# Kernel tuning notes

Measured on AMD Instinct MI355X. Metric: run time of the kernel, lower is better.

Reference implementation:

```python
import jax, jax.numpy as jnp
import numpy as np
from jax import lax

T, D, NH, CATS = 1024, 2048, 2048, 1000


def setup_inputs() -> dict:
    key = jax.random.key(0)
    ks = jax.random.split(key, 16)
    s = 0.02
    return {
        "x": jax.random.normal(ks[0], (T, D), dtype=jnp.float32),
        "Wh": jax.random.normal(ks[1], (NH, D), dtype=jnp.float32) * s,
        "Wz": jax.random.normal(ks[2], (NH, D), dtype=jnp.float32) * s,
        "Wr": jax.random.normal(ks[3], (NH, D), dtype=jnp.float32) * s,
        "Uh": jax.random.normal(ks[4], (NH, NH), dtype=jnp.float32) * s,
        "Uz": jax.random.normal(ks[5], (NH, NH), dtype=jnp.float32) * s,
        "bz": jax.random.normal(ks[6], (NH,), dtype=jnp.float32) * s,
        "Ur": jax.random.normal(ks[7], (NH, NH), dtype=jnp.float32) * s,
        "br": jax.random.normal(ks[8], (NH,), dtype=jnp.float32) * s,
        "Wout": jax.random.normal(ks[9], (CATS, NH), dtype=jnp.float32) * s,
        "h0": jax.random.normal(ks[10], (NH,), dtype=jnp.float32),
        "zt0": jax.random.normal(ks[11], (NH,), dtype=jnp.float32),
        "htilde0": jax.random.normal(ks[12], (NH,), dtype=jnp.float32),
        "hprev0": jax.random.normal(ks[13], (NH,), dtype=jnp.float32),
    }


def reference(x, Wh, Wz, Wr, Uh, Uz, bz, Ur, br, Wout, h0, zt0, htilde0, hprev0):
    # Batch the input projections over all timesteps: [T,d] @ [d,nh] -> [T,nh]
    xh = x @ Wh.T
    xz = x @ Wz.T
    xr = x @ Wr.T

    # Faithful to the original update ORDER: h is computed from the *stale*
    # zt/htilde (from the previous iteration), then gates are refreshed.
    # The original's hadamard(a, b) = linear(a, diag(b)) is exactly a * b.
    def step(carry, xs):
        h, zt, htilde, hprev = carry
        xh_t, xz_t, xr_t = xs
        h_new = (1.0 - zt) * hprev + zt * htilde
        zt_new = jax.nn.sigmoid(xz_t + hprev @ Uz.T + bz)
        htilde_new = jnp.tanh(xh_t + hprev @ Uh.T)
        # rt = sigmoid(xr_t + hprev @ Ur.T + br)  # computed in original, never used
        return (h_new, zt_new, htilde_new, h_new), None

    (h_fin, _, _, _), _ = lax.scan(step, (h0, zt0, htilde0, hprev0), (xh, xz, xr))
    logits = h_fin @ Wout.T  # [cats]
    return jax.nn.softmax(logits, axis=0)
```

## Files before the change

kernel.cpp:

```cpp
#include <hip/hip_runtime.h>
#include <math.h>

#define TT  1024
#define DD  2048
#define NHH 2048
#define CC  1000

__global__ __launch_bounds__(256) void k_gemm(const float* __restrict__ X,
                                              const float* __restrict__ Wh,
                                              const float* __restrict__ Wz,
                                              const float* __restrict__ bz,
                                              float* __restrict__ XH,
                                              float* __restrict__ XZ) {
    __shared__ float As[32][68];
    __shared__ float Bs[32][68];
    const int z = blockIdx.z;
    const float* __restrict__ W = z ? Wz : Wh;
    float* __restrict__ OUT = z ? XZ : XH;
    const int n0 = blockIdx.x * 64;
    const int m0 = blockIdx.y * 64;
    const int tid = threadIdx.x;
    const int tx = tid & 15, ty = tid >> 4;
    const int lr = tid >> 2;
    const int lc = (tid & 3) * 8;

    float acc[4][4] = {};
    for (int k0 = 0; k0 < DD; k0 += 32) {
        float4 a0 = *(const float4*)&X[(size_t)(m0 + lr) * DD + k0 + lc];
        float4 a1 = *(const float4*)&X[(size_t)(m0 + lr) * DD + k0 + lc + 4];
        float4 b0 = *(const float4*)&W[(size_t)(n0 + lr) * DD + k0 + lc];
        float4 b1 = *(const float4*)&W[(size_t)(n0 + lr) * DD + k0 + lc + 4];
        As[lc+0][lr]=a0.x; As[lc+1][lr]=a0.y; As[lc+2][lr]=a0.z; As[lc+3][lr]=a0.w;
        As[lc+4][lr]=a1.x; As[lc+5][lr]=a1.y; As[lc+6][lr]=a1.z; As[lc+7][lr]=a1.w;
        Bs[lc+0][lr]=b0.x; Bs[lc+1][lr]=b0.y; Bs[lc+2][lr]=b0.z; Bs[lc+3][lr]=b0.w;
        Bs[lc+4][lr]=b1.x; Bs[lc+5][lr]=b1.y; Bs[lc+6][lr]=b1.z; Bs[lc+7][lr]=b1.w;
        __syncthreads();
#pragma unroll
        for (int kk = 0; kk < 32; ++kk) {
            float4 av = *(const float4*)&As[kk][ty * 4];
            float4 bv = *(const float4*)&Bs[kk][tx * 4];
            acc[0][0] = fmaf(av.x, bv.x, acc[0][0]); acc[0][1] = fmaf(av.x, bv.y, acc[0][1]);
            acc[0][2] = fmaf(av.x, bv.z, acc[0][2]); acc[0][3] = fmaf(av.x, bv.w, acc[0][3]);
            acc[1][0] = fmaf(av.y, bv.x, acc[1][0]); acc[1][1] = fmaf(av.y, bv.y, acc[1][1]);
            acc[1][2] = fmaf(av.y, bv.z, acc[1][2]); acc[1][3] = fmaf(av.y, bv.w, acc[1][3]);
            acc[2][0] = fmaf(av.z, bv.x, acc[2][0]); acc[2][1] = fmaf(av.z, bv.y, acc[2][1]);
            acc[2][2] = fmaf(av.z, bv.z, acc[2][2]); acc[2][3] = fmaf(av.z, bv.w, acc[2][3]);
            acc[3][0] = fmaf(av.w, bv.x, acc[3][0]); acc[3][1] = fmaf(av.w, bv.y, acc[3][1]);
            acc[3][2] = fmaf(av.w, bv.z, acc[3][2]); acc[3][3] = fmaf(av.w, bv.w, acc[3][3]);
        }
        __syncthreads();
    }
    float4 bias = make_float4(0.f, 0.f, 0.f, 0.f);
    if (z) bias = *(const float4*)&bz[n0 + tx * 4];
#pragma unroll
    for (int i = 0; i < 4; ++i) {
        float4 o = make_float4(acc[i][0] + bias.x, acc[i][1] + bias.y,
                               acc[i][2] + bias.z, acc[i][3] + bias.w);
        *(float4*)&OUT[(size_t)(m0 + ty * 4 + i) * NHH + n0 + tx * 4] = o;
    }
}

__global__ __launch_bounds__(256, 1) void k_recur(
    const float* __restrict__ XH, const float* __restrict__ XZ,
    const float* __restrict__ Uh, const float* __restrict__ Uz,
    const float* __restrict__ zt0, const float* __restrict__ ht0,
    const float* __restrict__ hp0,
    unsigned long long* __restrict__ Hbuf) {
    __shared__ float Hs[NHH];
    __shared__ float dot_s[16];
    const int tid  = threadIdx.x;
    const int wave = tid >> 6, lane = tid & 63;
    const int base8 = blockIdx.x * 8;

    const float* __restrict__ Um = (wave < 2) ? Uz : Uh;
    const int r0 = base8 + (wave & 1) * 4;
    float u[4][32];
#pragma unroll
    for (int r = 0; r < 4; ++r) {
        const float* __restrict__ row = Um + (size_t)(r0 + r) * NHH;
#pragma unroll
        for (int c = 0; c < 8; ++c) {
            float4 v = *(const float4*)&row[c * 256 + lane * 4];
            u[r][c*4+0] = v.x; u[r][c*4+1] = v.y; u[r][c*4+2] = v.z; u[r][c*4+3] = v.w;
        }
    }
#pragma unroll
    for (int k = 0; k < 8; ++k) Hs[k * 256 + tid] = hp0[k * 256 + tid];

    float p_cur = 0.f;
    if (tid < 8) {
        float z0 = zt0[base8 + tid], g0 = ht0[base8 + tid], p0 = hp0[base8 + tid];
        p_cur = (1.0f - z0) * p0 + z0 * g0;
        unsigned long long pr = (1ull << 32) | (unsigned long long)__float_as_uint(p_cur);
        __hip_atomic_store(&Hbuf[(size_t)1 * NHH + base8 + tid], pr,
                           __ATOMIC_RELAXED, __HIP_MEMORY_SCOPE_SYSTEM);
    }
    __syncthreads();

    for (int t = 1; t < TT; ++t) {
        const unsigned long long* __restrict__ src = Hbuf + (size_t)(t & 3) * NHH;
        unsigned long long pv[8];
#pragma unroll
        for (int k = 0; k < 8; ++k)
            pv[k] = __hip_atomic_load(&src[k * 256 + tid], __ATOMIC_RELAXED, __HIP_MEMORY_SCOPE_SYSTEM);
        float xzv = 0.f, xhv = 0.f;
        if (tid < 8) {
            xzv = XZ[(size_t)(t - 1) * NHH + base8 + tid];
            xhv = XH[(size_t)(t - 1) * NHH + base8 + tid];
        }
        float a0 = 0.f, a1 = 0.f, a2 = 0.f, a3 = 0.f;
#pragma unroll
        for (int c = 0; c < 8; ++c) {
            float4 h4 = *(const float4*)&Hs[c * 256 + lane * 4];
            a0 = fmaf(u[0][c*4+0], h4.x, fmaf(u[0][c*4+1], h4.y, fmaf(u[0][c*4+2], h4.z, fmaf(u[0][c*4+3], h4.w, a0))));
            a1 = fmaf(u[1][c*4+0], h4.x, fmaf(u[1][c*4+1], h4.y, fmaf(u[1][c*4+2], h4.z, fmaf(u[1][c*4+3], h4.w, a1))));
            a2 = fmaf(u[2][c*4+0], h4.x, fmaf(u[2][c*4+1], h4.y, fmaf(u[2][c*4+2], h4.z, fmaf(u[2][c*4+3], h4.w, a2))));
            a3 = fmaf(u[3][c*4+0], h4.x, fmaf(u[3][c*4+1], h4.y, fmaf(u[3][c*4+2], h4.z, fmaf(u[3][c*4+3], h4.w, a3))));
        }
#pragma unroll
        for (int off = 32; off > 0; off >>= 1) {
            a0 += __shfl_xor(a0, off);
            a1 += __shfl_xor(a1, off);
            a2 += __shfl_xor(a2, off);
            a3 += __shfl_xor(a3, off);
        }
        if (lane == 0) {
            int di = ((wave & 1) * 4) + ((wave >> 1) * 8);
            dot_s[di + 0] = a0; dot_s[di + 1] = a1; dot_s[di + 2] = a2; dot_s[di + 3] = a3;
        }
        __syncthreads();
        if (tid < 8) {
            float z = 1.0f / (1.0f + expf(-(xzv + dot_s[tid])));
            float g = tanhf(xhv + dot_s[8 + tid]);
            float pn = (1.0f - z) * p_cur + z * g;
            p_cur = pn;
            unsigned long long pr = ((unsigned long long)(unsigned)(t + 1) << 32)
                                  | (unsigned long long)__float_as_uint(pn);
            __hip_atomic_store(&Hbuf[(size_t)((t + 1) & 3) * NHH + base8 + tid], pr,
                               __ATOMIC_RELAXED, __HIP_MEMORY_SCOPE_SYSTEM);
        }
        for (;;) {
            unsigned stale = 0;
#pragma unroll
            for (int k = 0; k < 8; ++k)
                if ((unsigned)(pv[k] >> 32) != (unsigned)t) stale |= (1u << k);
            if (!stale) break;
#pragma unroll
            for (int k = 0; k < 8; ++k)
                if (stale & (1u << k))
                    pv[k] = __hip_atomic_load(&src[k * 256 + tid], __ATOMIC_RELAXED, __HIP_MEMORY_SCOPE_SYSTEM);
        }
#pragma unroll
        for (int k = 0; k < 8; ++k) Hs[k * 256 + tid] = __uint_as_float((unsigned)pv[k]);
        __syncthreads();
    }
}

__global__ __launch_bounds__(256) void k_logits(const unsigned long long* __restrict__ Hbuf,
                                                const float* __restrict__ Wout,
                                                float* __restrict__ lg) {
    __shared__ float Hs[NHH];
    const int tid = threadIdx.x;
    for (int k = tid; k < NHH; k += 256) Hs[k] = __uint_as_float((unsigned)Hbuf[k]);
    __syncthreads();
    const int wave = tid >> 6, lane = tid & 63;
    const int row = blockIdx.x * 4 + wave;
    float a = 0.f;
#pragma unroll
    for (int c = 0; c < 8; ++c) {
        float4 w = *(const float4*)&Wout[(size_t)row * NHH + c * 256 + lane * 4];
        float4 h = *(const float4*)&Hs[c * 256 + lane * 4];
        a = fmaf(w.x, h.x, fmaf(w.y, h.y, fmaf(w.z, h.z, fmaf(w.w, h.w, a))));
    }
#pragma unroll
    for (int off = 32; off > 0; off >>= 1) a += __shfl_xor(a, off);
    if (lane == 0) lg[row] = a;
}

__global__ __launch_bounds__(1024) void k_softmax(const float* __restrict__ lg,
                                                  float* __restrict__ out) {
    const int i = threadIdx.x;
    __shared__ float red[16];
    __shared__ float bc[2];
    float v = (i < CC) ? lg[i] : -3.0e38f;
    float m = v;
#pragma unroll
    for (int off = 32; off > 0; off >>= 1) m = fmaxf(m, __shfl_xor(m, off));
    if ((i & 63) == 0) red[i >> 6] = m;
    __syncthreads();
    if (i == 0) { float mm = red[0]; for (int k = 1; k < 16; ++k) mm = fmaxf(mm, red[k]); bc[0] = mm; }
    __syncthreads();
    float e = (i < CC) ? expf(v - bc[0]) : 0.f;
    float s = e;
#pragma unroll
    for (int off = 32; off > 0; off >>= 1) s += __shfl_xor(s, off);
    if ((i & 63) == 0) red[i >> 6] = s;
    __syncthreads();
    if (i == 0) { float ss = 0.f; for (int k = 0; k < 16; ++k) ss += red[k]; bc[1] = ss; }
    __syncthreads();
    if (i < CC) out[i] = e / bc[1];
}

extern "C" void kernel_launch(void* const* d_in, const int* in_sizes, int n_in,
                              void* d_out, int out_size, void* d_ws, size_t ws_size,
                              hipStream_t stream) {
    const float* x    = (const float*)d_in[0];
    const float* Wh   = (const float*)d_in[1];
    const float* Wz   = (const float*)d_in[2];
    const float* Uh   = (const float*)d_in[4];
    const float* Uz   = (const float*)d_in[5];
    const float* bz   = (const float*)d_in[6];
    const float* Wout = (const float*)d_in[9];
    const float* zt0  = (const float*)d_in[11];
    const float* ht0  = (const float*)d_in[12];
    const float* hp0  = (const float*)d_in[13];
    float* out = (float*)d_out;

    float* XH = (float*)d_ws;
    float* XZ = XH + (size_t)TT * NHH;
    unsigned long long* Hbuf = (unsigned long long*)(XZ + (size_t)TT * NHH);
    float* lg = (float*)(Hbuf + 4 * NHH);

    k_gemm<<<dim3(NHH / 64, TT / 64, 2), dim3(256), 0, stream>>>(x, Wh, Wz, bz, XH, XZ);
    k_recur<<<dim3(256), dim3(256), 0, stream>>>(XH, XZ, Uh, Uz, zt0, ht0, hp0, Hbuf);
    k_logits<<<dim3(250), dim3(256), 0, stream>>>(Hbuf, Wout, lg);
    k_softmax<<<dim3(1), dim3(1024), 0, stream>>>(lg, out);
}
```

Before: 2.037 ms.

## Enlarge GEMM tiles to 128x128 with 8x8 register blocking and register prefetch

The input-projection GEMM now uses 128x128 output tiles with each thread computing an 8x8 micro-tile instead of 4x4, which raises arithmetic intensity per shared-memory load. It also prefetches the next K-slice from global memory into registers while the current slice is being computed, overlapping load latency with math. The grid shrinks to 256 blocks, which may under-fill the GPU's compute units, and the larger accumulator array raises register pressure. The total runtime is likely dominated by the sequential recurrence kernel, which this change does not touch.

```diff
diff --git a/kernel.cpp b/kernel.cpp
--- a/kernel.cpp
+++ b/kernel.cpp
@@ -12,51 +12,69 @@
                                               const float* __restrict__ bz,
                                               float* __restrict__ XH,
                                               float* __restrict__ XZ) {
-    __shared__ float As[32][68];
-    __shared__ float Bs[32][68];
+    __shared__ float As[32][132];
+    __shared__ float Bs[32][132];
     const int z = blockIdx.z;
     const float* __restrict__ W = z ? Wz : Wh;
     float* __restrict__ OUT = z ? XZ : XH;
-    const int n0 = blockIdx.x * 64;
-    const int m0 = blockIdx.y * 64;
+    const int n0 = blockIdx.x * 128;
+    const int m0 = blockIdx.y * 128;
     const int tid = threadIdx.x;
     const int tx = tid & 15, ty = tid >> 4;
-    const int lr = tid >> 2;
-    const int lc = (tid & 3) * 8;
-
-    float acc[4][4] = {};
+    const int lr = tid >> 1;
+    const int lq = (tid & 1) * 16;
+
+    float4 pa[4], pb[4];
+#pragma unroll
+    for (int q = 0; q < 4; ++q) {
+        pa[q] = *(const float4*)&X[(size_t)(m0 + lr) * DD + lq + q * 4];
+        pb[q] = *(const float4*)&W[(size_t)(n0 + lr) * DD + lq + q * 4];
+    }
+    float acc[8][8] = {};
     for (int k0 = 0; k0 < DD; k0 += 32) {
-        float4 a0 = *(const float4*)&X[(size_t)(m0 + lr) * DD + k0 + lc];
-        float4 a1 = *(const float4*)&X[(size_t)(m0 + lr) * DD + k0 + lc + 4];
-        float4 b0 = *(const float4*)&W[(size_t)(n0 + lr) * DD + k0 + lc];
-        float4 b1 = *(const float4*)&W[(size_t)(n0 + lr) * DD + k0 + lc + 4];
-        As[lc+0][lr]=a0.x; As[lc+1][lr]=a0.y; As[lc+2][lr]=a0.z; As[lc+3][lr]=a0.w;
-        As[lc+4][lr]=a1.x; As[lc+5][lr]=a1.y; As[lc+6][lr]=a1.z; As[lc+7][lr]=a1.w;
-        Bs[lc+0][lr]=b0.x; Bs[lc+1][lr]=b0.y; Bs[lc+2][lr]=b0.z; Bs[lc+3][lr]=b0.w;
-        Bs[lc+4][lr]=b1.x; Bs[lc+5][lr]=b1.y; Bs[lc+6][lr]=b1.z; Bs[lc+7][lr]=b1.w;
-        __syncthreads();
+#pragma unroll
+        for (int q = 0; q < 4; ++q) {
+            const int kc = lq + q * 4;
+            As[kc+0][lr]=pa[q].x; As[kc+1][lr]=pa[q].y; As[kc+2][lr]=pa[q].z; As[kc+3][lr]=pa[q].w;
+            Bs[kc+0][lr]=pb[q].x; Bs[kc+1][lr]=pb[q].y; Bs[kc+2][lr]=pb[q].z; Bs[kc+3][lr]=pb[q].w;
+        }
+        __syncthreads();
+        if (k0 + 32 < DD) {
+#pragma unroll
+            for (int q = 0; q < 4; ++q) {
+                pa[q] = *(const float4*)&X[(size_t)(m0 + lr) * DD + k0 + 32 + lq + q * 4];
+                pb[q] = *(const float4*)&W[(size_t)(n0 + lr) * DD + k0 + 32 + lq + q * 4];
+            }
+        }
 #pragma unroll
         for (int kk = 0; kk < 32; ++kk) {
-            float4 av = *(const float4*)&As[kk][ty * 4];
-            float4 bv = *(const float4*)&Bs[kk][tx * 4];
-            acc[0][0] = fmaf(av.x, bv.x, acc[0][0]); acc[0][1] = fmaf(av.x, bv.y, acc[0][1]);
-            acc[0][2] = fmaf(av.x, bv.z, acc[0][2]); acc[0][3] = fmaf(av.x, bv.w, acc[0][3]);
-            acc[1][0] = fmaf(av.y, bv.x, acc[1][0]); acc[1][1] = fmaf(av.y, bv.y, acc[1][1]);
-            acc[1][2] = fmaf(av.y, bv.z, acc[1][2]); acc[1][3] = fmaf(av.y, bv.w, acc[1][3]);
-            acc[2][0] = fmaf(av.z, bv.x, acc[2][0]); acc[2][1] = fmaf(av.z, bv.y, acc[2][1]);
-            acc[2][2] = fmaf(av.z, bv.z, acc[2][2]); acc[2][3] = fmaf(av.z, bv.w, acc[2][3]);
-            acc[3][0] = fmaf(av.w, bv.x, acc[3][0]); acc[3][1] = fmaf(av.w, bv.y, acc[3][1]);
-            acc[3][2] = fmaf(av.w, bv.z, acc[3][2]); acc[3][3] = fmaf(av.w, bv.w, acc[3][3]);
-        }
-        __syncthreads();
-    }
-    float4 bias = make_float4(0.f, 0.f, 0.f, 0.f);
-    if (z) bias = *(const float4*)&bz[n0 + tx * 4];
-#pragma unroll
-    for (int i = 0; i < 4; ++i) {
-        float4 o = make_float4(acc[i][0] + bias.x, acc[i][1] + bias.y,
-                               acc[i][2] + bias.z, acc[i][3] + bias.w);
-        *(float4*)&OUT[(size_t)(m0 + ty * 4 + i) * NHH + n0 + tx * 4] = o;
+            float4 a0 = *(const float4*)&As[kk][ty * 8];
+            float4 a1 = *(const float4*)&As[kk][ty * 8 + 4];
+            float4 b0 = *(const float4*)&Bs[kk][tx * 8];
+            float4 b1 = *(const float4*)&Bs[kk][tx * 8 + 4];
+            float a[8] = {a0.x,a0.y,a0.z,a0.w,a1.x,a1.y,a1.z,a1.w};
+            float b[8] = {b0.x,b0.y,b0.z,b0.w,b1.x,b1.y,b1.z,b1.w};
+#pragma unroll
+            for (int i = 0; i < 8; ++i)
+#pragma unroll
+                for (int j = 0; j < 8; ++j)
+                    acc[i][j] = fmaf(a[i], b[j], acc[i][j]);
+        }
+        __syncthreads();
+    }
+    float4 bias0 = make_float4(0.f,0.f,0.f,0.f), bias1 = bias0;
+    if (z) {
+        bias0 = *(const float4*)&bz[n0 + tx * 8];
+        bias1 = *(const float4*)&bz[n0 + tx * 8 + 4];
+    }
+#pragma unroll
+    for (int i = 0; i < 8; ++i) {
+        float4 o0 = make_float4(acc[i][0]+bias0.x, acc[i][1]+bias0.y,
+                                acc[i][2]+bias0.z, acc[i][3]+bias0.w);
+        float4 o1 = make_float4(acc[i][4]+bias1.x, acc[i][5]+bias1.y,
+                                acc[i][6]+bias1.z, acc[i][7]+bias1.w);
+        *(float4*)&OUT[(size_t)(m0 + ty * 8 + i) * NHH + n0 + tx * 8] = o0;
+        *(float4*)&OUT[(size_t)(m0 + ty * 8 + i) * NHH + n0 + tx * 8 + 4] = o1;
     }
 }
 
@@ -221,7 +239,7 @@
     unsigned long long* Hbuf = (unsigned long long*)(XZ + (size_t)TT * NHH);
     float* lg = (float*)(Hbuf + 4 * NHH);
 
-    k_gemm<<<dim3(NHH / 64, TT / 64, 2), dim3(256), 0, stream>>>(x, Wh, Wz, bz, XH, XZ);
+    k_gemm<<<dim3(NHH / 128, TT / 128, 2), dim3(256), 0, stream>>>(x, Wh, Wz, bz, XH, XZ);
     k_recur<<<dim3(256), dim3(256), 0, stream>>>(XH, XZ, Uh, Uz, zt0, ht0, hp0, Hbuf);
     k_logits<<<dim3(250), dim3(256), 0, stream>>>(Hbuf, Wout, lg);
     k_softmax<<<dim3(1), dim3(1024), 0, stream>>>(lg, out);
```

After: 2.033 ms (median of 2 runs). Within noise of the previous version (-0.2%).

## Fuse input projection GEMM into persistent recurrence kernel, overlapping with spin-wait

Applied to the files above, without the earlier changes.

Drops the separate k_gemm launch and computes each block's 8 rows of the Wz/Wh input projection inside the recurrent kernel. The block keeps its Wz/Wh rows resident in LDS (128 KB) and computes the next timestep's projection from x while it waits for the other blocks' hidden-state publication. This removes the GEMM kernel and the XH/XZ workspace round trip, and hides the projection work in the sync latency. The cost is more LDS per block and extra work per step in the serial loop, which could lengthen the step if it is not fully hidden.

```diff
diff --git a/kernel.cpp b/kernel.cpp
--- a/kernel.cpp
+++ b/kernel.cpp
@@ -6,68 +6,18 @@
 #define NHH 2048
 #define CC  1000
 
-__global__ __launch_bounds__(256) void k_gemm(const float* __restrict__ X,
-                                              const float* __restrict__ Wh,
-                                              const float* __restrict__ Wz,
-                                              const float* __restrict__ bz,
-                                              float* __restrict__ XH,
-                                              float* __restrict__ XZ) {
-    __shared__ float As[32][68];
-    __shared__ float Bs[32][68];
-    const int z = blockIdx.z;
-    const float* __restrict__ W = z ? Wz : Wh;
-    float* __restrict__ OUT = z ? XZ : XH;
-    const int n0 = blockIdx.x * 64;
-    const int m0 = blockIdx.y * 64;
-    const int tid = threadIdx.x;
-    const int tx = tid & 15, ty = tid >> 4;
-    const int lr = tid >> 2;
-    const int lc = (tid & 3) * 8;
-
-    float acc[4][4] = {};
-    for (int k0 = 0; k0 < DD; k0 += 32) {
-        float4 a0 = *(const float4*)&X[(size_t)(m0 + lr) * DD + k0 + lc];
-        float4 a1 = *(const float4*)&X[(size_t)(m0 + lr) * DD + k0 + lc + 4];
-        float4 b0 = *(const float4*)&W[(size_t)(n0 + lr) * DD + k0 + lc];
-        float4 b1 = *(const float4*)&W[(size_t)(n0 + lr) * DD + k0 + lc + 4];
-        As[lc+0][lr]=a0.x; As[lc+1][lr]=a0.y; As[lc+2][lr]=a0.z; As[lc+3][lr]=a0.w;
-        As[lc+4][lr]=a1.x; As[lc+5][lr]=a1.y; As[lc+6][lr]=a1.z; As[lc+7][lr]=a1.w;
-        Bs[lc+0][lr]=b0.x; Bs[lc+1][lr]=b0.y; Bs[lc+2][lr]=b0.z; Bs[lc+3][lr]=b0.w;
-        Bs[lc+4][lr]=b1.x; Bs[lc+5][lr]=b1.y; Bs[lc+6][lr]=b1.z; Bs[lc+7][lr]=b1.w;
-        __syncthreads();
-#pragma unroll
-        for (int kk = 0; kk < 32; ++kk) {
-            float4 av = *(const float4*)&As[kk][ty * 4];
-            float4 bv = *(const float4*)&Bs[kk][tx * 4];
-            acc[0][0] = fmaf(av.x, bv.x, acc[0][0]); acc[0][1] = fmaf(av.x, bv.y, acc[0][1]);
-            acc[0][2] = fmaf(av.x, bv.z, acc[0][2]); acc[0][3] = fmaf(av.x, bv.w, acc[0][3]);
-            acc[1][0] = fmaf(av.y, bv.x, acc[1][0]); acc[1][1] = fmaf(av.y, bv.y, acc[1][1]);
-            acc[1][2] = fmaf(av.y, bv.z, acc[1][2]); acc[1][3] = fmaf(av.y, bv.w, acc[1][3]);
-            acc[2][0] = fmaf(av.z, bv.x, acc[2][0]); acc[2][1] = fmaf(av.z, bv.y, acc[2][1]);
-            acc[2][2] = fmaf(av.z, bv.z, acc[2][2]); acc[2][3] = fmaf(av.z, bv.w, acc[2][3]);
-            acc[3][0] = fmaf(av.w, bv.x, acc[3][0]); acc[3][1] = fmaf(av.w, bv.y, acc[3][1]);
-            acc[3][2] = fmaf(av.w, bv.z, acc[3][2]); acc[3][3] = fmaf(av.w, bv.w, acc[3][3]);
-        }
-        __syncthreads();
-    }
-    float4 bias = make_float4(0.f, 0.f, 0.f, 0.f);
-    if (z) bias = *(const float4*)&bz[n0 + tx * 4];
-#pragma unroll
-    for (int i = 0; i < 4; ++i) {
-        float4 o = make_float4(acc[i][0] + bias.x, acc[i][1] + bias.y,
-                               acc[i][2] + bias.z, acc[i][3] + bias.w);
-        *(float4*)&OUT[(size_t)(m0 + ty * 4 + i) * NHH + n0 + tx * 4] = o;
-    }
-}
-
 __global__ __launch_bounds__(256, 1) void k_recur(
-    const float* __restrict__ XH, const float* __restrict__ XZ,
+    const float* __restrict__ X,
+    const float* __restrict__ Wh, const float* __restrict__ Wz,
+    const float* __restrict__ bz,
     const float* __restrict__ Uh, const float* __restrict__ Uz,
     const float* __restrict__ zt0, const float* __restrict__ ht0,
     const float* __restrict__ hp0,
     unsigned long long* __restrict__ Hbuf) {
+    __shared__ float Wlds[16][DD];
     __shared__ float Hs[NHH];
     __shared__ float dot_s[16];
+    __shared__ float xp_s[2][16];
     const int tid  = threadIdx.x;
     const int wave = tid >> 6, lane = tid & 63;
     const int base8 = blockIdx.x * 8;
@@ -84,30 +34,66 @@
             u[r][c*4+0] = v.x; u[r][c*4+1] = v.y; u[r][c*4+2] = v.z; u[r][c*4+3] = v.w;
         }
     }
+
+#pragma unroll
+    for (int j = 0; j < 8; ++j) {
+        const float* __restrict__ rz = Wz + (size_t)(base8 + j) * DD;
+        const float* __restrict__ rh = Wh + (size_t)(base8 + j) * DD;
+        *(float4*)&Wlds[j][tid * 8]         = *(const float4*)&rz[tid * 8];
+        *(float4*)&Wlds[j][tid * 8 + 4]     = *(const float4*)&rz[tid * 8 + 4];
+        *(float4*)&Wlds[8 + j][tid * 8]     = *(const float4*)&rh[tid * 8];
+        *(float4*)&Wlds[8 + j][tid * 8 + 4] = *(const float4*)&rh[tid * 8 + 4];
+    }
+
 #pragma unroll
     for (int k = 0; k < 8; ++k) Hs[k * 256 + tid] = hp0[k * 256 + tid];
-
-    float p_cur = 0.f;
+    float p_cur = 0.f, bz_r = 0.f;
     if (tid < 8) {
         float z0 = zt0[base8 + tid], g0 = ht0[base8 + tid], p0 = hp0[base8 + tid];
         p_cur = (1.0f - z0) * p0 + z0 * g0;
+        bz_r = bz[base8 + tid];
         unsigned long long pr = (1ull << 32) | (unsigned long long)__float_as_uint(p_cur);
         __hip_atomic_store(&Hbuf[(size_t)1 * NHH + base8 + tid], pr,
                            __ATOMIC_RELAXED, __HIP_MEMORY_SCOPE_SYSTEM);
     }
     __syncthreads();
 
+    {
+        const int j0 = ((wave >> 1) * 8) + (wave & 1) * 4;
+        const float4* __restrict__ xrow = (const float4*)X;
+        float a0 = 0.f, a1 = 0.f, a2 = 0.f, a3 = 0.f;
+#pragma unroll
+        for (int c = 0; c < 8; ++c) {
+            float4 xv = xrow[c * 64 + lane];
+            float4 w0 = *(const float4*)&Wlds[j0 + 0][c * 256 + lane * 4];
+            float4 w1 = *(const float4*)&Wlds[j0 + 1][c * 256 + lane * 4];
+            float4 w2 = *(const float4*)&Wlds[j0 + 2][c * 256 + lane * 4];
+            float4 w3 = *(const float4*)&Wlds[j0 + 3][c * 256 + lane * 4];
+            a0 = fmaf(w0.x, xv.x, fmaf(w0.y, xv.y, fmaf(w0.z, xv.z, fmaf(w0.w, xv.w, a0))));
+            a1 = fmaf(w1.x, xv.x, fmaf(w1.y, xv.y, fmaf(w1.z, xv.z, fmaf(w1.w, xv.w, a1))));
+            a2 = fmaf(w2.x, xv.x, fmaf(w2.y, xv.y, fmaf(w2.z, xv.z, fmaf(w2.w, xv.w, a2))));
+            a3 = fmaf(w3.x, xv.x, fmaf(w3.y, xv.y, fmaf(w3.z, xv.z, fmaf(w3.w, xv.w, a3))));
+        }
+#pragma unroll
+        for (int off = 32; off > 0; off >>= 1) {
+            a0 += __shfl_xor(a0, off); a1 += __shfl_xor(a1, off);
+            a2 += __shfl_xor(a2, off); a3 += __shfl_xor(a3, off);
+        }
+        if (lane == 0) {
+            int di = ((wave & 1) * 4) + ((wave >> 1) * 8);
+            xp_s[1][di + 0] = a0; xp_s[1][di + 1] = a1;
+            xp_s[1][di + 2] = a2; xp_s[1][di + 3] = a3;
+        }
+    }
+    __syncthreads();
+
     for (int t = 1; t < TT; ++t) {
         const unsigned long long* __restrict__ src = Hbuf + (size_t)(t & 3) * NHH;
         unsigned long long pv[8];
 #pragma unroll
         for (int k = 0; k < 8; ++k)
             pv[k] = __hip_atomic_load(&src[k * 256 + tid], __ATOMIC_RELAXED, __HIP_MEMORY_SCOPE_SYSTEM);
-        float xzv = 0.f, xhv = 0.f;
-        if (tid < 8) {
-            xzv = XZ[(size_t)(t - 1) * NHH + base8 + tid];
-            xhv = XH[(size_t)(t - 1) * NHH + base8 + tid];
-        }
+
         float a0 = 0.f, a1 = 0.f, a2 = 0.f, a3 = 0.f;
 #pragma unroll
         for (int c = 0; c < 8; ++c) {
@@ -119,19 +105,18 @@
         }
 #pragma unroll
         for (int off = 32; off > 0; off >>= 1) {
-            a0 += __shfl_xor(a0, off);
-            a1 += __shfl_xor(a1, off);
-            a2 += __shfl_xor(a2, off);
-            a3 += __shfl_xor(a3, off);
+            a0 += __shfl_xor(a0, off); a1 += __shfl_xor(a1, off);
+            a2 += __shfl_xor(a2, off); a3 += __shfl_xor(a3, off);
         }
         if (lane == 0) {
             int di = ((wave & 1) * 4) + ((wave >> 1) * 8);
             dot_s[di + 0] = a0; dot_s[di + 1] = a1; dot_s[di + 2] = a2; dot_s[di + 3] = a3;
         }
         __syncthreads();
+
         if (tid < 8) {
-            float z = 1.0f / (1.0f + expf(-(xzv + dot_s[tid])));
-            float g = tanhf(xhv + dot_s[8 + tid]);
+            float z = 1.0f / (1.0f + expf(-(xp_s[t & 1][tid] + bz_r + dot_s[tid])));
+            float g = tanhf(xp_s[t & 1][8 + tid] + dot_s[8 + tid]);
             float pn = (1.0f - z) * p_cur + z * g;
             p_cur = pn;
             unsigned long long pr = ((unsigned long long)(unsigned)(t + 1) << 32)
@@ -139,6 +124,35 @@
             __hip_atomic_store(&Hbuf[(size_t)((t + 1) & 3) * NHH + base8 + tid], pr,
                                __ATOMIC_RELAXED, __HIP_MEMORY_SCOPE_SYSTEM);
         }
+
+        if (t < TT - 1) {
+            const int j0 = ((wave >> 1) * 8) + (wave & 1) * 4;
+            const float4* __restrict__ xrow = (const float4*)(X + (size_t)t * DD);
+            float b0 = 0.f, b1 = 0.f, b2 = 0.f, b3 = 0.f;
+#pragma unroll
+            for (int c = 0; c < 8; ++c) {
+                float4 xv = xrow[c * 64 + lane];
+                float4 w0 = *(const float4*)&Wlds[j0 + 0][c * 256 + lane * 4];
+                float4 w1 = *(const float4*)&Wlds[j0 + 1][c * 256 + lane * 4];
+                float4 w2 = *(const float4*)&Wlds[j0 + 2][c * 256 + lane * 4];
+                float4 w3 = *(const float4*)&Wlds[j0 + 3][c * 256 + lane * 4];
+                b0 = fmaf(w0.x, xv.x, fmaf(w0.y, xv.y, fmaf(w0.z, xv.z, fmaf(w0.w, xv.w, b0))));
+                b1 = fmaf(w1.x, xv.x, fmaf(w1.y, xv.y, fmaf(w1.z, xv.z, fmaf(w1.w, xv.w, b1))));
+                b2 = fmaf(w2.x, xv.x, fmaf(w2.y, xv.y, fmaf(w2.z, xv.z, fmaf(w2.w, xv.w, b2))));
+                b3 = fmaf(w3.x, xv.x, fmaf(w3.y, xv.y, fmaf(w3.z, xv.z, fmaf(w3.w, xv.w, b3))));
+            }
+#pragma unroll
+            for (int off = 32; off > 0; off >>= 1) {
+                b0 += __shfl_xor(b0, off); b1 += __shfl_xor(b1, off);
+                b2 += __shfl_xor(b2, off); b3 += __shfl_xor(b3, off);
+            }
+            if (lane == 0) {
+                int di = ((wave & 1) * 4) + ((wave >> 1) * 8);
+                xp_s[(t + 1) & 1][di + 0] = b0; xp_s[(t + 1) & 1][di + 1] = b1;
+                xp_s[(t + 1) & 1][di + 2] = b2; xp_s[(t + 1) & 1][di + 3] = b3;
+            }
+        }
+
         for (;;) {
             unsigned stale = 0;
 #pragma unroll
@@ -216,13 +230,10 @@
     const float* hp0  = (const float*)d_in[13];
     float* out = (float*)d_out;
 
-    float* XH = (float*)d_ws;
-    float* XZ = XH + (size_t)TT * NHH;
-    unsigned long long* Hbuf = (unsigned long long*)(XZ + (size_t)TT * NHH);
+    unsigned long long* Hbuf = (unsigned long long*)d_ws;
     float* lg = (float*)(Hbuf + 4 * NHH);
 
-    k_gemm<<<dim3(NHH / 64, TT / 64, 2), dim3(256), 0, stream>>>(x, Wh, Wz, bz, XH, XZ);
-    k_recur<<<dim3(256), dim3(256), 0, stream>>>(XH, XZ, Uh, Uz, zt0, ht0, hp0, Hbuf);
+    k_recur<<<dim3(256), dim3(256), 0, stream>>>(x, Wh, Wz, bz, Uh, Uz, zt0, ht0, hp0, Hbuf);
     k_logits<<<dim3(250), dim3(256), 0, stream>>>(Hbuf, Wout, lg);
     k_softmax<<<dim3(1), dim3(1024), 0, stream>>>(lg, out);
 }
```

Result: slower. 3.665 ms (+80.0%).
